# Optimization experiments

Hardware: AMD Instinct MI355X
Metric: run time of the kernel (lower is better)

## Reference

```python
import jax, jax.numpy as jnp
import numpy as np

B = 16      # number of point clouds in the batch
N = 2048    # points per cloud
P = B * N   # total points (flat PyG-style batching)
K = 16      # neighbors per point (col 0 = self loop)
OUT = 512   # out_channels


def _linear(key, fi, fo):
    # torch nn.Linear default init: U(-1/sqrt(fi), 1/sqrt(fi))
    s = 1.0 / np.sqrt(fi)
    kw, kb = jax.random.split(key)
    W = jax.random.uniform(kw, (fi, fo), jnp.float32, -s, s)
    b = jax.random.uniform(kb, (fo,), jnp.float32, -s, s)
    return W, b


def setup_inputs() -> dict:
    key = jax.random.key(0)
    ks = jax.random.split(key, 6)
    pos = jax.random.normal(ks[0], (P, 3), jnp.float32)
    # flat batch vector: points are grouped contiguously per cloud
    batch = (jnp.arange(P, dtype=jnp.int32) // N).astype(jnp.int32)
    # within-cloud random neighbor indices (stand-in for knn/radius graph)
    base = (jnp.arange(P) // N) * N  # offset of each point's cloud
    nbr = base[:, None] + jax.random.randint(ks[1], (P, K), 0, N)
    nbr = nbr.at[:, 0].set(jnp.arange(P))  # self loop (PyG add_self_loops)
    W1, b1 = _linear(ks[2], 3, 64)          # sa1 MLP layer 1
    W2, b2 = _linear(ks[3], 64, 128)        # sa1 MLP layer 2
    W3, b3 = _linear(ks[4], 128 + 3, 256)   # sa2 MLP layer 1
    W4, b4 = _linear(ks[5], 256, OUT)       # sa2 MLP layer 2
    return dict(pos=pos, nbr=nbr.astype(jnp.int64), batch=batch,
                W1=W1, b1=b1, W2=W2, b2=b2, W3=W3, b3=b3, W4=W4, b4=b4)


def reference(pos, nbr, batch, W1, b1, W2, b2, W3, b3, W4, b4):
    # ----- sa1: x is None -> message = MLP(pos_j - pos_i), max-aggregated -----
    diff = pos[nbr] - pos[:, None, :]                      # [P, K, 3]
    h1 = jnp.maximum(diff @ W1 + b1, 0.0) @ W2 + b2        # [P, K, 128]
    x1 = jnp.max(h1, axis=1)                               # [P, 128]
    # ----- sa2: message = MLP([x1_j, pos_j - pos_i]), max-aggregated -----
    feats = jnp.concatenate([x1[nbr], diff], axis=-1)      # [P, K, 131]
    h2 = jnp.maximum(feats @ W3 + b3, 0.0) @ W4 + b4       # [P, K, 512]
    x2 = jnp.max(h2, axis=1)                               # [P, 512]
    # ----- global_max_pool over batch -----
    return jax.ops.segment_max(x2, batch, num_segments=B)  # [B, 512]
```

## Files before the change

### kernel.cpp

```cpp
#include <hip/hip_runtime.h>
#include <hip/hip_bf16.h>

#define PTOT   32768
#define KNB    16
#define NCLOUD 16
#define OUTC   512
#define A1S    168
#define A2S    264

typedef __attribute__((ext_vector_type(8)))  short v8bf;
typedef __attribute__((ext_vector_type(16))) float v16f;

__device__ __forceinline__ unsigned short f2b(float v) {
    __hip_bfloat16 h = __float2bfloat16(v);
    return *reinterpret_cast<unsigned short*>(&h);
}
__device__ __forceinline__ unsigned pk2(float a, float b) {
    return (unsigned)f2b(a) | ((unsigned)f2b(b) << 16);
}
__device__ __forceinline__ unsigned fenc(float f) {
    unsigned u = __float_as_uint(f);
    return (u & 0x80000000u) ? ~u : (u | 0x80000000u);
}
__device__ __forceinline__ float fdec(unsigned u) {
    unsigned b = (u & 0x80000000u) ? (u & 0x7FFFFFFFu) : ~u;
    return __uint_as_float(b);
}
__device__ __forceinline__ v16f zero16() {
    v16f z;
    #pragma unroll
    for (int i = 0; i < 16; ++i) z[i] = 0.0f;
    return z;
}

__global__ void prep_kernel(const float* __restrict__ W1, const float* __restrict__ W2,
                            const float* __restrict__ W3, const float* __restrict__ W4,
                            unsigned short* __restrict__ W1s, unsigned short* __restrict__ W2s,
                            unsigned short* __restrict__ W3s, unsigned short* __restrict__ W4s)
{
    int i = blockIdx.x * 256 + threadIdx.x;
    if (i < 40960) {
        int j = i & 7, n = (i >> 3) & 255, c2 = i >> 11;
        int k = c2 * 8 + j;
        W3s[i] = f2b(k < 131 ? W3[k * 256 + n] : 0.0f);
    }
    int i2 = i - 40960;
    if (i2 >= 0 && i2 < 131072) {
        int j = i2 & 7, n = (i2 >> 3) & 511, c2 = i2 >> 12;
        int k = c2 * 8 + j;
        W4s[i2] = f2b(W4[k * 512 + n]);
    }
    int i3 = i - 172032;
    if (i3 >= 0 && i3 < 1024) {
        int k = i3 & 15, n = i3 >> 4;
        W1s[i3] = f2b(k < 3 ? W1[k * 64 + n] : 0.0f);
    }
    int i4 = i - 173056;
    if (i4 >= 0 && i4 < 8192) {
        int k = i4 & 63, n = i4 >> 6;
        W2s[i4] = f2b(W2[k * 128 + n]);
    }
}

__global__ __launch_bounds__(256) void sa1_kernel(
    const float* __restrict__ pos, const int* __restrict__ nbr,
    const unsigned short* __restrict__ W1s, const float* __restrict__ b1,
    const unsigned short* __restrict__ W2s, const float* __restrict__ b2,
    unsigned short* __restrict__ x1b)
{
    __shared__ unsigned short A1d[64 * 16];
    __shared__ unsigned short A2[64 * 72];
    const int tid  = threadIdx.x;
    const int lane = tid & 63;
    const int wave = tid >> 6;
    const int l31  = lane & 31;
    const int h    = lane >> 5;
    const int p0   = blockIdx.x * 4;

    if (tid < 64) {
        int r = tid;
        int j = nbr[p0 * KNB + r];
        int p = p0 + (r >> 4);
        v8bf z;
        #pragma unroll
        for (int i = 0; i < 8; ++i) z[i] = 0;
        v8bf dv = z;
        dv[0] = (short)f2b(pos[j * 3 + 0] - pos[p * 3 + 0]);
        dv[1] = (short)f2b(pos[j * 3 + 1] - pos[p * 3 + 1]);
        dv[2] = (short)f2b(pos[j * 3 + 2] - pos[p * 3 + 2]);
        *(v8bf*)(A1d + r * 16)     = dv;
        *(v8bf*)(A1d + r * 16 + 8) = z;
    }
    const int c1 = (wave >> 1) * 32 + l31;
    v8bf b1f = *(const v8bf*)(W1s + c1 * 16 + h * 8);
    const float b1v = b1[c1];
    __syncthreads();

    {
        v8bf a = *(const v8bf*)(A1d + ((wave & 1) * 32 + l31) * 16 + h * 8);
        v16f acc = __builtin_amdgcn_mfma_f32_32x32x16_bf16(a, b1f, zero16(), 0, 0, 0);
        #pragma unroll
        for (int r = 0; r < 16; ++r) {
            int row = (wave & 1) * 32 + (r & 3) + 8 * (r >> 2) + 4 * h;
            A2[row * 72 + c1] = f2b(fmaxf(acc[r] + b1v, 0.0f));
        }
    }
    v8bf B2[4];
    #pragma unroll
    for (int kc = 0; kc < 4; ++kc)
        B2[kc] = *(const v8bf*)(W2s + (wave * 32 + l31) * 64 + kc * 16 + h * 8);
    const float b2v = b2[wave * 32 + l31];
    __syncthreads();

    #pragma unroll
    for (int rt = 0; rt < 2; ++rt) {
        v16f acc = zero16();
        #pragma unroll
        for (int kc = 0; kc < 4; ++kc) {
            v8bf a = *(const v8bf*)(A2 + (rt * 32 + l31) * 72 + kc * 16 + h * 8);
            acc = __builtin_amdgcn_mfma_f32_32x32x16_bf16(a, B2[kc], acc, 0, 0, 0);
        }
        float ma = acc[0], mb = acc[8];
        #pragma unroll
        for (int r = 1; r < 8; ++r) { ma = fmaxf(ma, acc[r]); mb = fmaxf(mb, acc[8 + r]); }
        ma = fmaxf(ma, __shfl_xor(ma, 32));
        mb = fmaxf(mb, __shfl_xor(mb, 32));
        int p = p0 + rt * 2 + h;
        float m = h ? mb : ma;
        x1b[p * 128 + wave * 32 + l31] = f2b(m + b2v);
    }
}

__global__ __launch_bounds__(512) void sa2_kernel(
    const float* __restrict__ pos, const int* __restrict__ nbr,
    const int* __restrict__ batch,
    const unsigned short* __restrict__ W3s, const float* __restrict__ b3,
    const unsigned short* __restrict__ W4s, const float* __restrict__ b4,
    const unsigned short* __restrict__ x1b, unsigned* __restrict__ encbuf)
{
    __shared__ unsigned short S[128 * A2S];
    const int tid  = threadIdx.x;
    const int lane = tid & 63;
    const int wave = tid >> 6;
    const int l31  = lane & 31;
    const int h    = lane >> 5;
    const int p0   = blockIdx.x * 8;
    const int rtp  = wave >> 2;
    const int cg   = wave & 3;

    {
        int r = tid >> 2, q4 = tid & 3;
        int j = nbr[p0 * KNB + r];
        const uint4* src = (const uint4*)(x1b + j * 128 + q4 * 32);
        uint4* dst = (uint4*)(S + r * A1S + q4 * 32);
        dst[0] = src[0]; dst[1] = src[1]; dst[2] = src[2]; dst[3] = src[3];
    }
    if (tid < 128) {
        int r = tid;
        int j = nbr[p0 * KNB + r];
        int p = p0 + (r >> 4);
        v8bf z;
        #pragma unroll
        for (int i = 0; i < 8; ++i) z[i] = 0;
        v8bf dv = z;
        dv[0] = (short)f2b(pos[j * 3 + 0] - pos[p * 3 + 0]);
        dv[1] = (short)f2b(pos[j * 3 + 1] - pos[p * 3 + 1]);
        dv[2] = (short)f2b(pos[j * 3 + 2] - pos[p * 3 + 2]);
        *(v8bf*)(S + r * A1S + 128) = dv;
        *(v8bf*)(S + r * A1S + 136) = z;
    }
    __syncthreads();

    const int rbase = rtp * 64;
    const int n1a = (cg * 2 + 0) * 32 + l31;
    const int n1b = (cg * 2 + 1) * 32 + l31;
    const float b3v0 = b3[n1a];
    const float b3v1 = b3[n1b];
    v16f g00 = zero16(), g01 = zero16(), g10 = zero16(), g11 = zero16();
    #pragma unroll
    for (int kc = 0; kc < 9; ++kc) {
        v8bf a0 = *(const v8bf*)(S + (rbase + l31)      * A1S + kc * 16 + h * 8);
        v8bf a1 = *(const v8bf*)(S + (rbase + 32 + l31) * A1S + kc * 16 + h * 8);
        int c2 = kc * 2 + h;
        v8bf B0 = *(const v8bf*)(W3s + ((c2 * 256 + n1a) << 3));
        v8bf B1 = *(const v8bf*)(W3s + ((c2 * 256 + n1b) << 3));
        g00 = __builtin_amdgcn_mfma_f32_32x32x16_bf16(a0, B0, g00, 0, 0, 0);
        g10 = __builtin_amdgcn_mfma_f32_32x32x16_bf16(a1, B0, g10, 0, 0, 0);
        g01 = __builtin_amdgcn_mfma_f32_32x32x16_bf16(a0, B1, g01, 0, 0, 0);
        g11 = __builtin_amdgcn_mfma_f32_32x32x16_bf16(a1, B1, g11, 0, 0, 0);
    }
    unsigned st00[8], st10[8], st01[8], st11[8];
    #pragma unroll
    for (int i = 0; i < 8; ++i) {
        st00[i] = pk2(fmaxf(g00[2*i] + b3v0, 0.0f), fmaxf(g00[2*i+1] + b3v0, 0.0f));
        st10[i] = pk2(fmaxf(g10[2*i] + b3v0, 0.0f), fmaxf(g10[2*i+1] + b3v0, 0.0f));
        st01[i] = pk2(fmaxf(g01[2*i] + b3v1, 0.0f), fmaxf(g01[2*i+1] + b3v1, 0.0f));
        st11[i] = pk2(fmaxf(g11[2*i] + b3v1, 0.0f), fmaxf(g11[2*i+1] + b3v1, 0.0f));
    }
    __syncthreads();

    #pragma unroll
    for (int i = 0; i < 8; ++i) {
        int row = rbase + ((2*i) & 3) + 8 * ((2*i) >> 2) + 4 * h;
        S[row * A2S + n1a]        = (unsigned short)(st00[i] & 0xFFFF);
        S[(row + 1) * A2S + n1a]  = (unsigned short)(st00[i] >> 16);
        S[(row + 32) * A2S + n1a] = (unsigned short)(st10[i] & 0xFFFF);
        S[(row + 33) * A2S + n1a] = (unsigned short)(st10[i] >> 16);
        S[row * A2S + n1b]        = (unsigned short)(st01[i] & 0xFFFF);
        S[(row + 1) * A2S + n1b]  = (unsigned short)(st01[i] >> 16);
        S[(row + 32) * A2S + n1b] = (unsigned short)(st11[i] & 0xFFFF);
        S[(row + 33) * A2S + n1b] = (unsigned short)(st11[i] >> 16);
    }
    __syncthreads();

    const int cloud = batch[p0];
    #pragma unroll
    for (int pass = 0; pass < 2; ++pass) {
        const int ct0 = cg * 4 + pass * 2;
        const int n0 = ct0 * 32 + l31;
        const int n1 = (ct0 + 1) * 32 + l31;
        v16f a00 = zero16(), a01 = zero16(), a10 = zero16(), a11 = zero16();
        #pragma unroll
        for (int kc = 0; kc < 16; ++kc) {
            v8bf a0 = *(const v8bf*)(S + (rbase + l31)      * A2S + kc * 16 + h * 8);
            v8bf a1 = *(const v8bf*)(S + (rbase + 32 + l31) * A2S + kc * 16 + h * 8);
            int c2 = kc * 2 + h;
            v8bf Ba = *(const v8bf*)(W4s + ((c2 * 512 + n0) << 3));
            v8bf Bb = *(const v8bf*)(W4s + ((c2 * 512 + n1) << 3));
            a00 = __builtin_amdgcn_mfma_f32_32x32x16_bf16(a0, Ba, a00, 0, 0, 0);
            a10 = __builtin_amdgcn_mfma_f32_32x32x16_bf16(a1, Ba, a10, 0, 0, 0);
            a01 = __builtin_amdgcn_mfma_f32_32x32x16_bf16(a0, Bb, a01, 0, 0, 0);
            a11 = __builtin_amdgcn_mfma_f32_32x32x16_bf16(a1, Bb, a11, 0, 0, 0);
        }
        float rm0 = -3.4e38f, rm1 = -3.4e38f;
        #pragma unroll
        for (int r = 0; r < 16; ++r) {
            rm0 = fmaxf(rm0, fmaxf(a00[r], a10[r]));
            rm1 = fmaxf(rm1, fmaxf(a01[r], a11[r]));
        }
        rm0 = fmaxf(rm0, __shfl_xor(rm0, 32));
        rm1 = fmaxf(rm1, __shfl_xor(rm1, 32));
        rm0 += b4[ct0 * 32 + l31];
        rm1 += b4[(ct0 + 1) * 32 + l31];
        if (lane < 32) {
            atomicMax(&encbuf[cloud * OUTC + ct0 * 32 + l31], fenc(rm0));
            atomicMax(&encbuf[cloud * OUTC + (ct0 + 1) * 32 + l31], fenc(rm1));
        }
    }
}

__global__ void finalize_kernel(const unsigned* __restrict__ encv,
                                float* __restrict__ out)
{
    int i = blockIdx.x * 256 + threadIdx.x;
    if (i < NCLOUD * OUTC) out[i] = fdec(encv[i]);
}

extern "C" void kernel_launch(void* const* d_in, const int* in_sizes, int n_in,
                              void* d_out, int out_size, void* d_ws, size_t ws_size,
                              hipStream_t stream)
{
    const float* pos   = (const float*)d_in[0];
    const int*   nbr   = (const int*)  d_in[1];
    const int*   batch = (const int*)  d_in[2];
    const float* W1    = (const float*)d_in[3];
    const float* b1    = (const float*)d_in[4];
    const float* W2    = (const float*)d_in[5];
    const float* b2    = (const float*)d_in[6];
    const float* W3    = (const float*)d_in[7];
    const float* b3    = (const float*)d_in[8];
    const float* W4    = (const float*)d_in[9];
    const float* b4    = (const float*)d_in[10];

    unsigned short* x1b = (unsigned short*)d_ws;
    unsigned short* W3s = (unsigned short*)((char*)d_ws + 8388608);
    unsigned short* W4s = (unsigned short*)((char*)d_ws + 8470528);
    unsigned*    encbuf = (unsigned*)((char*)d_ws + 8732672);
    unsigned short* W1s = (unsigned short*)((char*)d_ws + 8765440);
    unsigned short* W2s = (unsigned short*)((char*)d_ws + 8767488);

    hipMemsetAsync(encbuf, 0, NCLOUD * OUTC * sizeof(unsigned), stream);
    prep_kernel<<<708, 256, 0, stream>>>(W1, W2, W3, W4, W1s, W2s, W3s, W4s);
    sa1_kernel<<<PTOT / 4, 256, 0, stream>>>(pos, nbr, W1s, b1, W2s, b2, x1b);
    sa2_kernel<<<PTOT / 8, 512, 0, stream>>>(pos, nbr, batch, W3s, b3, W4s, b4, x1b, encbuf);
    finalize_kernel<<<(NCLOUD * OUTC + 255) / 256, 256, 0, stream>>>(encbuf, (float*)d_out);
}
```

Measured before the change: 262.7 us.

## Restructure sa1 to process 8 points per block with per-wave row tiles

The sa1 kernel now handles 8 points per block. Each wave owns 32 neighbor rows and builds its layer-1 A fragment directly in registers, which removes the A1d shared staging buffer and one barrier. Each wave then computes all 128 output columns for its rows, loading W2 fragments from global memory inside the loop. The encbuf zeroing moves from a memset into prep_kernel to save one launch. Half as many sa1 blocks are launched, but the W2 loads now sit on the inner loop and more LDS is used per block.

```diff
diff --git a/kernel.cpp b/kernel.cpp
--- a/kernel.cpp
+++ b/kernel.cpp
@@ -36,9 +36,11 @@
 __global__ void prep_kernel(const float* __restrict__ W1, const float* __restrict__ W2,
                             const float* __restrict__ W3, const float* __restrict__ W4,
                             unsigned short* __restrict__ W1s, unsigned short* __restrict__ W2s,
-                            unsigned short* __restrict__ W3s, unsigned short* __restrict__ W4s)
+                            unsigned short* __restrict__ W3s, unsigned short* __restrict__ W4s,
+                            unsigned* __restrict__ encbuf)
 {
     int i = blockIdx.x * 256 + threadIdx.x;
+    if (i < NCLOUD * OUTC) encbuf[i] = 0u;
     if (i < 40960) {
         int j = i & 7, n = (i >> 3) & 255, c2 = i >> 11;
         int k = c2 * 8 + j;
@@ -68,66 +70,69 @@
     const unsigned short* __restrict__ W2s, const float* __restrict__ b2,
     unsigned short* __restrict__ x1b)
 {
-    __shared__ unsigned short A1d[64 * 16];
-    __shared__ unsigned short A2[64 * 72];
+    __shared__ unsigned short A2[128 * 72];
     const int tid  = threadIdx.x;
     const int lane = tid & 63;
     const int wave = tid >> 6;
     const int l31  = lane & 31;
     const int h    = lane >> 5;
-    const int p0   = blockIdx.x * 4;
-
-    if (tid < 64) {
-        int r = tid;
-        int j = nbr[p0 * KNB + r];
-        int p = p0 + (r >> 4);
-        v8bf z;
-        #pragma unroll
-        for (int i = 0; i < 8; ++i) z[i] = 0;
-        v8bf dv = z;
-        dv[0] = (short)f2b(pos[j * 3 + 0] - pos[p * 3 + 0]);
-        dv[1] = (short)f2b(pos[j * 3 + 1] - pos[p * 3 + 1]);
-        dv[2] = (short)f2b(pos[j * 3 + 2] - pos[p * 3 + 2]);
-        *(v8bf*)(A1d + r * 16)     = dv;
-        *(v8bf*)(A1d + r * 16 + 8) = z;
-    }
-    const int c1 = (wave >> 1) * 32 + l31;
-    v8bf b1f = *(const v8bf*)(W1s + c1 * 16 + h * 8);
-    const float b1v = b1[c1];
-    __syncthreads();
-
-    {
-        v8bf a = *(const v8bf*)(A1d + ((wave & 1) * 32 + l31) * 16 + h * 8);
-        v16f acc = __builtin_amdgcn_mfma_f32_32x32x16_bf16(a, b1f, zero16(), 0, 0, 0);
-        #pragma unroll
-        for (int r = 0; r < 16; ++r) {
-            int row = (wave & 1) * 32 + (r & 3) + 8 * (r >> 2) + 4 * h;
-            A2[row * 72 + c1] = f2b(fmaxf(acc[r] + b1v, 0.0f));
-        }
-    }
-    v8bf B2[4];
-    #pragma unroll
-    for (int kc = 0; kc < 4; ++kc)
-        B2[kc] = *(const v8bf*)(W2s + (wave * 32 + l31) * 64 + kc * 16 + h * 8);
-    const float b2v = b2[wave * 32 + l31];
-    __syncthreads();
-
-    #pragma unroll
-    for (int rt = 0; rt < 2; ++rt) {
-        v16f acc = zero16();
+    const int p0   = blockIdx.x * 8;
+    const int rbase = wave * 32;
+
+    const int r = rbase + l31;
+    const int j = nbr[p0 * KNB + r];
+    const int p = p0 + (r >> 4);
+    v8bf afrag;
+    #pragma unroll
+    for (int i = 0; i < 8; ++i) afrag[i] = 0;
+    if (h == 0) {
+        afrag[0] = (short)f2b(pos[j * 3 + 0] - pos[p * 3 + 0]);
+        afrag[1] = (short)f2b(pos[j * 3 + 1] - pos[p * 3 + 1]);
+        afrag[2] = (short)f2b(pos[j * 3 + 2] - pos[p * 3 + 2]);
+    }
+
+    #pragma unroll
+    for (int ct = 0; ct < 2; ++ct) {
+        const int c = ct * 32 + l31;
+        v8bf b1f = *(const v8bf*)(W1s + c * 16 + h * 8);
+        v16f acc = __builtin_amdgcn_mfma_f32_32x32x16_bf16(afrag, b1f, zero16(), 0, 0, 0);
+        const float b1v = b1[c];
+        #pragma unroll
+        for (int i = 0; i < 8; ++i) {
+            unsigned pr = pk2(fmaxf(acc[2 * i] + b1v, 0.0f), fmaxf(acc[2 * i + 1] + b1v, 0.0f));
+            int row = rbase + ((2 * i) & 3) + 8 * ((2 * i) >> 2) + 4 * h;
+            A2[row * 72 + c]       = (unsigned short)(pr & 0xFFFF);
+            A2[(row + 1) * 72 + c] = (unsigned short)(pr >> 16);
+        }
+    }
+    __syncthreads();
+
+    #pragma unroll
+    for (int cp = 0; cp < 2; ++cp) {
+        const int c0 = (cp * 2 + 0) * 32 + l31;
+        const int c1 = (cp * 2 + 1) * 32 + l31;
+        v16f acc0 = zero16(), acc1 = zero16();
         #pragma unroll
         for (int kc = 0; kc < 4; ++kc) {
-            v8bf a = *(const v8bf*)(A2 + (rt * 32 + l31) * 72 + kc * 16 + h * 8);
-            acc = __builtin_amdgcn_mfma_f32_32x32x16_bf16(a, B2[kc], acc, 0, 0, 0);
-        }
-        float ma = acc[0], mb = acc[8];
-        #pragma unroll
-        for (int r = 1; r < 8; ++r) { ma = fmaxf(ma, acc[r]); mb = fmaxf(mb, acc[8 + r]); }
-        ma = fmaxf(ma, __shfl_xor(ma, 32));
-        mb = fmaxf(mb, __shfl_xor(mb, 32));
-        int p = p0 + rt * 2 + h;
-        float m = h ? mb : ma;
-        x1b[p * 128 + wave * 32 + l31] = f2b(m + b2v);
+            v8bf a  = *(const v8bf*)(A2 + (rbase + l31) * 72 + kc * 16 + h * 8);
+            v8bf Ba = *(const v8bf*)(W2s + c0 * 64 + kc * 16 + h * 8);
+            v8bf Bb = *(const v8bf*)(W2s + c1 * 64 + kc * 16 + h * 8);
+            acc0 = __builtin_amdgcn_mfma_f32_32x32x16_bf16(a, Ba, acc0, 0, 0, 0);
+            acc1 = __builtin_amdgcn_mfma_f32_32x32x16_bf16(a, Bb, acc1, 0, 0, 0);
+        }
+        float ma0 = acc0[0], mb0 = acc0[8], ma1 = acc1[0], mb1 = acc1[8];
+        #pragma unroll
+        for (int i = 1; i < 8; ++i) {
+            ma0 = fmaxf(ma0, acc0[i]); mb0 = fmaxf(mb0, acc0[8 + i]);
+            ma1 = fmaxf(ma1, acc1[i]); mb1 = fmaxf(mb1, acc1[8 + i]);
+        }
+        ma0 = fmaxf(ma0, __shfl_xor(ma0, 32)); mb0 = fmaxf(mb0, __shfl_xor(mb0, 32));
+        ma1 = fmaxf(ma1, __shfl_xor(ma1, 32)); mb1 = fmaxf(mb1, __shfl_xor(mb1, 32));
+        const int pw = p0 + wave * 2 + h;
+        float m0 = h ? mb0 : ma0;
+        float m1 = h ? mb1 : ma1;
+        x1b[pw * 128 + c0] = f2b(m0 + b2[c0]);
+        x1b[pw * 128 + c1] = f2b(m1 + b2[c1]);
     }
 }
 
@@ -234,9 +239,9 @@
         }
         float rm0 = -3.4e38f, rm1 = -3.4e38f;
         #pragma unroll
-        for (int r = 0; r < 16; ++r) {
-            rm0 = fmaxf(rm0, fmaxf(a00[r], a10[r]));
-            rm1 = fmaxf(rm1, fmaxf(a01[r], a11[r]));
+        for (int rr = 0; rr < 16; ++rr) {
+            rm0 = fmaxf(rm0, fmaxf(a00[rr], a10[rr]));
+            rm1 = fmaxf(rm1, fmaxf(a01[rr], a11[rr]));
         }
         rm0 = fmaxf(rm0, __shfl_xor(rm0, 32));
         rm1 = fmaxf(rm1, __shfl_xor(rm1, 32));
@@ -279,9 +284,8 @@
     unsigned short* W1s = (unsigned short*)((char*)d_ws + 8765440);
     unsigned short* W2s = (unsigned short*)((char*)d_ws + 8767488);
 
-    hipMemsetAsync(encbuf, 0, NCLOUD * OUTC * sizeof(unsigned), stream);
-    prep_kernel<<<708, 256, 0, stream>>>(W1, W2, W3, W4, W1s, W2s, W3s, W4s);
-    sa1_kernel<<<PTOT / 4, 256, 0, stream>>>(pos, nbr, W1s, b1, W2s, b2, x1b);
+    prep_kernel<<<708, 256, 0, stream>>>(W1, W2, W3, W4, W1s, W2s, W3s, W4s, encbuf);
+    sa1_kernel<<<PTOT / 8, 256, 0, stream>>>(pos, nbr, W1s, b1, W2s, b2, x1b);
     sa2_kernel<<<PTOT / 8, 512, 0, stream>>>(pos, nbr, batch, W3s, b3, W4s, b4, x1b, encbuf);
     finalize_kernel<<<(NCLOUD * OUTC + 255) / 256, 256, 0, stream>>>(encbuf, (float*)d_out);
 }
```

Result: slower. 280.2 us (+6.7%).
